# Performance work log

Measured on AMD Instinct MI355X. Metric: run time of the kernel, lower is better.

Reference implementation:

```python
import jax, jax.numpy as jnp
import numpy as np

NH = 8       # num_heads
EDIM = 256   # embedding_dim (also per-head dim in this module)
BS, SQL = 4, 1024


def setup_inputs() -> dict:
    key = jax.random.key(0)
    ks = jax.random.split(key, 5)
    scale_in = 1.0 / np.sqrt(EDIM)
    scale_out = 1.0 / np.sqrt(NH * EDIM)
    return {
        "x": jax.random.normal(ks[0], (BS, SQL, EDIM), dtype=jnp.float32),
        "w_attn": jax.random.normal(ks[1], (NH * 3 * EDIM, EDIM), dtype=jnp.float32) * scale_in,
        "b_attn": jax.random.normal(ks[2], (NH * 3 * EDIM,), dtype=jnp.float32) * scale_in,
        "w_out": jax.random.normal(ks[3], (EDIM, NH * EDIM), dtype=jnp.float32) * scale_out,
        "b_out": jax.random.normal(ks[4], (EDIM,), dtype=jnp.float32) * scale_out,
    }


def reference(x, w_attn, b_attn, w_out, b_out):
    bs, sql, edim = x.shape
    nh = NH
    # projections: (bs, sql, nh*3*edim); split into Q, K, V chunks of nh*edim
    proj = x @ w_attn.T + b_attn
    q, k, v = jnp.split(proj, 3, axis=-1)
    # Faithful to torch: raw view (bs, sql, nh*edim) -> (bs, nh, sql, edim),
    # a reinterpretation of memory, NOT a transpose.
    q = q.reshape(bs, nh, sql, edim)
    k = k.reshape(bs, nh, sql, edim)
    v = v.reshape(bs, nh, sql, edim)
    # scaled dot-product scores: (bs, nh, sql, sql)
    scores = jnp.einsum("bhqd,bhkd->bhqk", q, k) / jnp.sqrt(jnp.float32(edim))
    # causal mask: -inf strictly above the diagonal (equivalent to adding triu(-inf, 1))
    causal = jnp.tril(jnp.ones((sql, sql), dtype=bool))
    scores = jnp.where(causal, scores, -jnp.inf)
    attn = jax.nn.softmax(scores, axis=-1)
    out = jnp.einsum("bhqk,bhkd->bhqd", attn, v)
    # Faithful raw view back: (bs, nh, sql, edim) -> (bs, sql, nh*edim)
    out = out.reshape(bs, sql, nh * edim)
    return out @ w_out.T + b_out
```

## Files before the change

kernel.cpp:

```cpp
#include <hip/hip_runtime.h>

#define SQL  1024
#define EDIM 256
#define NHD  8
#define NKV  (NHD * 3 * EDIM)
#define MROWS (4 * SQL)

typedef short bf16x8 __attribute__((ext_vector_type(8)));
typedef float f32x4 __attribute__((ext_vector_type(4)));

__device__ __forceinline__ unsigned short f2bf(float f) {
  unsigned u = __float_as_uint(f);
  u += 0x7fff + ((u >> 16) & 1);
  return (unsigned short)(u >> 16);
}

__device__ __forceinline__ void g2lds16(const void* g, void* l) {
  __builtin_amdgcn_global_load_lds(
      (const __attribute__((address_space(1))) unsigned int*)g,
      (__attribute__((address_space(3))) unsigned int*)l, 16, 0, 0);
}

__device__ __forceinline__ void storev(float* p, float v) { *p = v; }
__device__ __forceinline__ void storev(unsigned short* p, float v) { *p = f2bf(v); }

__global__ __launch_bounds__(256) void cast_bf16(
    const float* __restrict__ in, unsigned short* __restrict__ out, int n8) {
  int i = blockIdx.x * 256 + threadIdx.x;
  if (i >= n8) return;
  float4 a = ((const float4*)in)[2 * i];
  float4 b = ((const float4*)in)[2 * i + 1];
  union { unsigned short s[8]; ulonglong2 v; } u;
  u.s[0] = f2bf(a.x); u.s[1] = f2bf(a.y); u.s[2] = f2bf(a.z); u.s[3] = f2bf(a.w);
  u.s[4] = f2bf(b.x); u.s[5] = f2bf(b.y); u.s[6] = f2bf(b.z); u.s[7] = f2bf(b.w);
  ((ulonglong2*)out)[i] = u.v;
}

template <int BM, int BN, typename OutT>
__global__ __launch_bounds__(256) void gemm_mfma(
    const unsigned short* __restrict__ A, const unsigned short* __restrict__ B,
    const float* __restrict__ bias, OutT* __restrict__ C,
    int M, int N, int K) {
  constexpr int TM = BM / 32, TN = BN / 32;
  __shared__ __align__(16) unsigned short As[2][BM * 32];
  __shared__ __align__(16) unsigned short Bs[2][BN * 32];
  const int tid = threadIdx.x;
  const int wave = tid >> 6, lane = tid & 63;
  const int quad = lane >> 4, l16 = lane & 15;
  const int wm = (wave >> 1) * (BM / 2), wn = (wave & 1) * (BN / 2);
  const int m0 = blockIdx.x * BM, n0 = blockIdx.y * BN;
  const int sw = (l16 >> 1) & 3;

  f32x4 acc[TM][TN];
  #pragma unroll
  for (int i = 0; i < TM; i++)
    #pragma unroll
    for (int j = 0; j < TN; j++) acc[i][j] = {0.f, 0.f, 0.f, 0.f};

  auto stage = [&](int k0, int bb) {
    #pragma unroll
    for (int it = 0; it < BM / 64; it++) {
      int flat = it * 256 + tid;
      int row = flat >> 2;
      int cg = (flat & 3) ^ ((row >> 1) & 3);
      g2lds16(A + (size_t)(m0 + row) * K + k0 + cg * 8, &As[bb][flat * 8]);
    }
    #pragma unroll
    for (int it = 0; it < BN / 64; it++) {
      int flat = it * 256 + tid;
      int row = flat >> 2;
      int cg = (flat & 3) ^ ((row >> 1) & 3);
      g2lds16(B + (size_t)(n0 + row) * K + k0 + cg * 8, &Bs[bb][flat * 8]);
    }
  };

  stage(0, 0);
  __syncthreads();
  for (int k0 = 0; k0 < K; k0 += 32) {
    const int bb = (k0 >> 5) & 1;
    if (k0 + 32 < K) stage(k0 + 32, bb ^ 1);
    bf16x8 af[TM], bf[TN];
    #pragma unroll
    for (int i = 0; i < TM; i++)
      af[i] = *(const bf16x8*)&As[bb][(wm + i * 16 + l16) * 32 + (quad ^ sw) * 8];
    #pragma unroll
    for (int j = 0; j < TN; j++)
      bf[j] = *(const bf16x8*)&Bs[bb][(wn + j * 16 + l16) * 32 + (quad ^ sw) * 8];
    #pragma unroll
    for (int i = 0; i < TM; i++)
      #pragma unroll
      for (int j = 0; j < TN; j++)
        acc[i][j] = __builtin_amdgcn_mfma_f32_16x16x32_bf16(af[i], bf[j], acc[i][j], 0, 0, 0);
    __syncthreads();
  }

  #pragma unroll
  for (int i = 0; i < TM; i++) {
    #pragma unroll
    for (int r = 0; r < 4; r++) {
      int m = m0 + wm + i * 16 + quad * 4 + r;
      #pragma unroll
      for (int j = 0; j < TN; j++) {
        int n = n0 + wn + j * 16 + l16;
        storev(&C[(size_t)m * N + n], acc[i][j][r] + bias[n]);
      }
    }
  }
}

__global__ __launch_bounds__(256) void transpose_v(
    const unsigned short* __restrict__ proj, unsigned short* __restrict__ vt) {
  __shared__ unsigned short T[64][66];
  const int tid = threadIdx.x;
  const int s0 = blockIdx.x * 64, d0 = blockIdx.y * 64, bh = blockIdx.z;
  const int b = bh >> 3, h = bh & 7;
  #pragma unroll
  for (int it = 0; it < 2; it++) {
    int c = it * 256 + tid;
    int sr = c >> 3, k8 = (c & 7) * 8;
    int s = s0 + sr;
    const unsigned short* src = proj + (size_t)(b * SQL + h * 128 + (s >> 3)) * NKV
                                + 2 * 2048 + (s & 7) * 256 + d0 + k8;
    *(ulonglong2*)&T[sr][k8] = *(const ulonglong2*)src;
  }
  __syncthreads();
  #pragma unroll
  for (int it = 0; it < 2; it++) {
    int c = it * 256 + tid;
    int dr = c >> 3, s8 = (c & 7) * 8;
    unsigned short tmp[8];
    #pragma unroll
    for (int j = 0; j < 8; j++) tmp[j] = T[s8 + j][dr];
    unsigned short* dst = vt + ((size_t)bh * EDIM + d0 + dr) * SQL + s0 + s8;
    *(ulonglong2*)dst = *(ulonglong2*)tmp;
  }
}

__global__ __launch_bounds__(256) void attn_mfma(
    const unsigned short* __restrict__ proj,
    const unsigned short* __restrict__ vt,
    unsigned short* __restrict__ oflat) {
  __shared__ __align__(16) unsigned short lds[35328];
  unsigned short* Ps = lds + 32768;

  const int tid = threadIdx.x;
  const int wave = tid >> 6, lane = tid & 63;
  const int quad = lane >> 4, l16 = lane & 15;
  const int slot = blockIdx.x & 255, round = blockIdx.x >> 8;
  const int bh = slot & 31;
  const int j = slot >> 5;
  const int qt = round ? j : 15 - j;
  const int b = bh >> 3, h = bh & 7;
  const int q0 = qt * 64;

  #pragma unroll
  for (int it = 0; it < 8; it++) {
    int c = it * 256 + tid;
    int r = c >> 5, ch = (c & 31) ^ (r & 7);
    int s = q0 + r;
    g2lds16(proj + (size_t)(b * SQL + h * 128 + (s >> 3)) * NKV + (s & 7) * 256 + ch * 8,
            lds + c * 8);
  }
  __syncthreads();
  bf16x8 aq[8];
  const int qrow = wave * 16 + l16;
  #pragma unroll
  for (int kk = 0; kk < 8; kk++)
    aq[kk] = *(const bf16x8*)&lds[qrow * 256 + ((kk * 4 + quad) ^ (qrow & 7)) * 8];
  __syncthreads();

  f32x4 o[16];
  #pragma unroll
  for (int t = 0; t < 16; t++) o[t] = {0.f, 0.f, 0.f, 0.f};
  float l_r[4] = {0.f, 0.f, 0.f, 0.f};

  auto stage = [&](int kt, int bb) {
    unsigned short* KsB = lds + bb * 16384;
    unsigned short* VtB = KsB + 8192;
    #pragma unroll
    for (int it = 0; it < 4; it++) {
      int c = it * 256 + tid;
      int r = c >> 5, ch = (c & 31) ^ (r & 7);
      int s = kt * 32 + r;
      g2lds16(proj + (size_t)(b * SQL + h * 128 + (s >> 3)) * NKV + 2048 + (s & 7) * 256 + ch * 8,
              KsB + c * 8);
    }
    #pragma unroll
    for (int it = 0; it < 4; it++) {
      int c = it * 256 + tid;
      int d = c >> 2, ch = (c & 3) ^ (d & 3);
      g2lds16(vt + ((size_t)bh * EDIM + d) * SQL + kt * 32 + ch * 8, VtB + c * 8);
    }
  };

  const int nkt = 2 * qt + 2;
  stage(0, 0);
  __syncthreads();

  for (int kt = 0; kt < nkt; kt++) {
    const int bb = kt & 1;
    if (kt + 1 < nkt) stage(kt + 1, bb ^ 1);
    const unsigned short* KsB = lds + bb * 16384;
    const unsigned short* VtB = KsB + 8192;

    f32x4 s0 = {0.f, 0.f, 0.f, 0.f}, s1 = {0.f, 0.f, 0.f, 0.f};
    #pragma unroll
    for (int kk = 0; kk < 8; kk++) {
      int ch = (kk * 4 + quad) ^ (l16 & 7);
      bf16x8 b0 = *(const bf16x8*)&KsB[l16 * 256 + ch * 8];
      bf16x8 b1 = *(const bf16x8*)&KsB[(16 + l16) * 256 + ch * 8];
      s0 = __builtin_amdgcn_mfma_f32_16x16x32_bf16(aq[kk], b0, s0, 0, 0, 0);
      s1 = __builtin_amdgcn_mfma_f32_16x16x32_bf16(aq[kk], b1, s1, 0, 0, 0);
    }

    const int kg0 = kt * 32 + l16, kg1 = kg0 + 16;
    #pragma unroll
    for (int r = 0; r < 4; r++) {
      int qg = q0 + wave * 16 + quad * 4 + r;
      float p0 = (kg0 <= qg) ? __expf(s0[r] * 0.0625f) : 0.f;
      float p1 = (kg1 <= qg) ? __expf(s1[r] * 0.0625f) : 0.f;
      l_r[r] += p0 + p1;
      Ps[(wave * 16 + quad * 4 + r) * 40 + l16]      = f2bf(p0);
      Ps[(wave * 16 + quad * 4 + r) * 40 + 16 + l16] = f2bf(p1);
    }

    bf16x8 ap = *(const bf16x8*)&Ps[(wave * 16 + l16) * 40 + quad * 8];
    #pragma unroll
    for (int t = 0; t < 16; t++) {
      bf16x8 bv = *(const bf16x8*)&VtB[(t * 16 + l16) * 32 + (quad ^ (l16 & 3)) * 8];
      o[t] = __builtin_amdgcn_mfma_f32_16x16x32_bf16(ap, bv, o[t], 0, 0, 0);
    }
    __syncthreads();
  }

  #pragma unroll
  for (int r = 0; r < 4; r++) {
    float l = l_r[r];
    #pragma unroll
    for (int off = 1; off < 16; off <<= 1) l += __shfl_xor(l, off);
    float inv = 1.0f / l;
    int s = q0 + wave * 16 + quad * 4 + r;
    unsigned short* dst = oflat + (size_t)(b * SQL + h * 128 + (s >> 3)) * 2048 + (s & 7) * 256;
    #pragma unroll
    for (int t = 0; t < 16; t++)
      dst[t * 16 + l16] = f2bf(o[t][r] * inv);
  }
}

extern "C" void kernel_launch(void* const* d_in, const int* in_sizes, int n_in,
                              void* d_out, int out_size, void* d_ws, size_t ws_size,
                              hipStream_t stream) {
  const float* x      = (const float*)d_in[0];
  const float* w_attn = (const float*)d_in[1];
  const float* b_attn = (const float*)d_in[2];
  const float* w_out  = (const float*)d_in[3];
  const float* b_out  = (const float*)d_in[4];
  float* out = (float*)d_out;

  char* p = (char*)d_ws;
  unsigned short* proj = (unsigned short*)p;  p += (size_t)MROWS * NKV * 2;
  unsigned short* obf  = (unsigned short*)p;  p += (size_t)MROWS * 2048 * 2;
  unsigned short* vtb  = (unsigned short*)p;  p += (size_t)32 * EDIM * SQL * 2;
  unsigned short* xb   = (unsigned short*)p;  p += (size_t)MROWS * EDIM * 2;
  unsigned short* wb   = (unsigned short*)p;  p += (size_t)NKV * EDIM * 2;
  unsigned short* wob  = (unsigned short*)p;

  cast_bf16<<<(MROWS * EDIM / 8 + 255) / 256, 256, 0, stream>>>(x, xb, MROWS * EDIM / 8);
  cast_bf16<<<(NKV * EDIM / 8 + 255) / 256, 256, 0, stream>>>(w_attn, wb, NKV * EDIM / 8);
  cast_bf16<<<(EDIM * 2048 / 8 + 255) / 256, 256, 0, stream>>>(w_out, wob, EDIM * 2048 / 8);

  gemm_mfma<128, 128, unsigned short><<<dim3(MROWS / 128, NKV / 128), 256, 0, stream>>>(
      xb, wb, b_attn, proj, MROWS, NKV, EDIM);
  transpose_v<<<dim3(SQL / 64, EDIM / 64, 32), 256, 0, stream>>>(proj, vtb);
  attn_mfma<<<512, 256, 0, stream>>>(proj, vtb, obf);
  gemm_mfma<64, 64, float><<<dim3(MROWS / 64, EDIM / 64), 256, 0, stream>>>(
      obf, wob, b_out, out, MROWS, EDIM, NHD * EDIM);
}
```

Measured before the change: 170.9 us.

## Split attention head dim across wave pairs, skip masked tiles, fuse cast kernels

The attention kernel now runs 8 waves per block, with each pair of waves sharing a 16-row query strip and splitting the 256-wide output dimension into two halves. This halves the O accumulator registers per wave and doubles the waves available to hide latency. Waves whose query strip lies entirely before a key tile skip its compute. The exp is rewritten as exp2 with a folded scale constant, and the three fp32-to-bf16 cast launches are merged into one kernel to cut launch overhead. The trade-off is that QK^T is computed twice per query strip, once by each wave of the pair.

```diff
diff --git a/kernel.cpp b/kernel.cpp
--- a/kernel.cpp
+++ b/kernel.cpp
@@ -24,16 +24,21 @@
 __device__ __forceinline__ void storev(float* p, float v) { *p = v; }
 __device__ __forceinline__ void storev(unsigned short* p, float v) { *p = f2bf(v); }
 
-__global__ __launch_bounds__(256) void cast_bf16(
-    const float* __restrict__ in, unsigned short* __restrict__ out, int n8) {
+__global__ __launch_bounds__(256) void cast3_bf16(
+    const float* __restrict__ s0, unsigned short* __restrict__ d0, int n0,
+    const float* __restrict__ s1, unsigned short* __restrict__ d1, int n1,
+    const float* __restrict__ s2, unsigned short* __restrict__ d2, int n2) {
   int i = blockIdx.x * 256 + threadIdx.x;
-  if (i >= n8) return;
-  float4 a = ((const float4*)in)[2 * i];
-  float4 b = ((const float4*)in)[2 * i + 1];
-  union { unsigned short s[8]; ulonglong2 v; } u;
-  u.s[0] = f2bf(a.x); u.s[1] = f2bf(a.y); u.s[2] = f2bf(a.z); u.s[3] = f2bf(a.w);
-  u.s[4] = f2bf(b.x); u.s[5] = f2bf(b.y); u.s[6] = f2bf(b.z); u.s[7] = f2bf(b.w);
-  ((ulonglong2*)out)[i] = u.v;
+  const float* s; unsigned short* d;
+  if (i < n0) { s = s0; d = d0; }
+  else if (i < n0 + n1) { i -= n0; s = s1; d = d1; }
+  else { i -= n0 + n1; if (i >= n2) return; s = s2; d = d2; }
+  float4 a = ((const float4*)s)[2 * i];
+  float4 b = ((const float4*)s)[2 * i + 1];
+  union { unsigned short u[8]; ulonglong2 v; } t;
+  t.u[0] = f2bf(a.x); t.u[1] = f2bf(a.y); t.u[2] = f2bf(a.z); t.u[3] = f2bf(a.w);
+  t.u[4] = f2bf(b.x); t.u[5] = f2bf(b.y); t.u[6] = f2bf(b.z); t.u[7] = f2bf(b.w);
+  ((ulonglong2*)d)[i] = t.v;
 }
 
 template <int BM, int BN, typename OutT>
@@ -136,26 +141,28 @@
   }
 }
 
-__global__ __launch_bounds__(256) void attn_mfma(
+__global__ __launch_bounds__(512, 4) void attn_mfma(
     const unsigned short* __restrict__ proj,
     const unsigned short* __restrict__ vt,
     unsigned short* __restrict__ oflat) {
-  __shared__ __align__(16) unsigned short lds[35328];
+  __shared__ __align__(16) unsigned short lds[37888];
   unsigned short* Ps = lds + 32768;
 
   const int tid = threadIdx.x;
   const int wave = tid >> 6, lane = tid & 63;
   const int quad = lane >> 4, l16 = lane & 15;
+  const int qs = wave >> 1;
+  const int dh = wave & 1;
   const int slot = blockIdx.x & 255, round = blockIdx.x >> 8;
   const int bh = slot & 31;
-  const int j = slot >> 5;
-  const int qt = round ? j : 15 - j;
+  const int jj = slot >> 5;
+  const int qt = round ? jj : 15 - jj;
   const int b = bh >> 3, h = bh & 7;
   const int q0 = qt * 64;
 
   #pragma unroll
-  for (int it = 0; it < 8; it++) {
-    int c = it * 256 + tid;
+  for (int it = 0; it < 4; it++) {
+    int c = it * 512 + tid;
     int r = c >> 5, ch = (c & 31) ^ (r & 7);
     int s = q0 + r;
     g2lds16(proj + (size_t)(b * SQL + h * 128 + (s >> 3)) * NKV + (s & 7) * 256 + ch * 8,
@@ -163,31 +170,31 @@
   }
   __syncthreads();
   bf16x8 aq[8];
-  const int qrow = wave * 16 + l16;
+  const int qrow = qs * 16 + l16;
   #pragma unroll
   for (int kk = 0; kk < 8; kk++)
     aq[kk] = *(const bf16x8*)&lds[qrow * 256 + ((kk * 4 + quad) ^ (qrow & 7)) * 8];
   __syncthreads();
 
-  f32x4 o[16];
-  #pragma unroll
-  for (int t = 0; t < 16; t++) o[t] = {0.f, 0.f, 0.f, 0.f};
+  f32x4 o[8];
+  #pragma unroll
+  for (int t = 0; t < 8; t++) o[t] = {0.f, 0.f, 0.f, 0.f};
   float l_r[4] = {0.f, 0.f, 0.f, 0.f};
 
   auto stage = [&](int kt, int bb) {
     unsigned short* KsB = lds + bb * 16384;
     unsigned short* VtB = KsB + 8192;
     #pragma unroll
-    for (int it = 0; it < 4; it++) {
-      int c = it * 256 + tid;
+    for (int it = 0; it < 2; it++) {
+      int c = it * 512 + tid;
       int r = c >> 5, ch = (c & 31) ^ (r & 7);
       int s = kt * 32 + r;
       g2lds16(proj + (size_t)(b * SQL + h * 128 + (s >> 3)) * NKV + 2048 + (s & 7) * 256 + ch * 8,
               KsB + c * 8);
     }
     #pragma unroll
-    for (int it = 0; it < 4; it++) {
-      int c = it * 256 + tid;
+    for (int it = 0; it < 2; it++) {
+      int c = it * 512 + tid;
       int d = c >> 2, ch = (c & 3) ^ (d & 3);
       g2lds16(vt + ((size_t)bh * EDIM + d) * SQL + kt * 32 + ch * 8, VtB + c * 8);
     }
@@ -202,33 +209,38 @@
     if (kt + 1 < nkt) stage(kt + 1, bb ^ 1);
     const unsigned short* KsB = lds + bb * 16384;
     const unsigned short* VtB = KsB + 8192;
-
-    f32x4 s0 = {0.f, 0.f, 0.f, 0.f}, s1 = {0.f, 0.f, 0.f, 0.f};
-    #pragma unroll
-    for (int kk = 0; kk < 8; kk++) {
-      int ch = (kk * 4 + quad) ^ (l16 & 7);
-      bf16x8 b0 = *(const bf16x8*)&KsB[l16 * 256 + ch * 8];
-      bf16x8 b1 = *(const bf16x8*)&KsB[(16 + l16) * 256 + ch * 8];
-      s0 = __builtin_amdgcn_mfma_f32_16x16x32_bf16(aq[kk], b0, s0, 0, 0, 0);
-      s1 = __builtin_amdgcn_mfma_f32_16x16x32_bf16(aq[kk], b1, s1, 0, 0, 0);
-    }
-
-    const int kg0 = kt * 32 + l16, kg1 = kg0 + 16;
-    #pragma unroll
-    for (int r = 0; r < 4; r++) {
-      int qg = q0 + wave * 16 + quad * 4 + r;
-      float p0 = (kg0 <= qg) ? __expf(s0[r] * 0.0625f) : 0.f;
-      float p1 = (kg1 <= qg) ? __expf(s1[r] * 0.0625f) : 0.f;
-      l_r[r] += p0 + p1;
-      Ps[(wave * 16 + quad * 4 + r) * 40 + l16]      = f2bf(p0);
-      Ps[(wave * 16 + quad * 4 + r) * 40 + 16 + l16] = f2bf(p1);
-    }
-
-    bf16x8 ap = *(const bf16x8*)&Ps[(wave * 16 + l16) * 40 + quad * 8];
-    #pragma unroll
-    for (int t = 0; t < 16; t++) {
-      bf16x8 bv = *(const bf16x8*)&VtB[(t * 16 + l16) * 32 + (quad ^ (l16 & 3)) * 8];
-      o[t] = __builtin_amdgcn_mfma_f32_16x16x32_bf16(ap, bv, o[t], 0, 0, 0);
+    const bool live = (kt * 32 <= q0 + qs * 16 + 15);
+
+    if (live) {
+      f32x4 s0 = {0.f, 0.f, 0.f, 0.f}, s1 = {0.f, 0.f, 0.f, 0.f};
+      #pragma unroll
+      for (int kk = 0; kk < 8; kk++) {
+        int ch = (kk * 4 + quad) ^ (l16 & 7);
+        bf16x8 b0 = *(const bf16x8*)&KsB[l16 * 256 + ch * 8];
+        bf16x8 b1 = *(const bf16x8*)&KsB[(16 + l16) * 256 + ch * 8];
+        s0 = __builtin_amdgcn_mfma_f32_16x16x32_bf16(aq[kk], b0, s0, 0, 0, 0);
+        s1 = __builtin_amdgcn_mfma_f32_16x16x32_bf16(aq[kk], b1, s1, 0, 0, 0);
+      }
+
+      const int kg0 = kt * 32 + l16, kg1 = kg0 + 16;
+      unsigned short* PsW = Ps + wave * 640;
+      #pragma unroll
+      for (int r = 0; r < 4; r++) {
+        int qg = q0 + qs * 16 + quad * 4 + r;
+        float p0 = (kg0 <= qg) ? exp2f(s0[r] * 0.09016844f) : 0.f;
+        float p1 = (kg1 <= qg) ? exp2f(s1[r] * 0.09016844f) : 0.f;
+        l_r[r] += p0 + p1;
+        PsW[(quad * 4 + r) * 40 + l16]      = f2bf(p0);
+        PsW[(quad * 4 + r) * 40 + 16 + l16] = f2bf(p1);
+      }
+
+      bf16x8 ap = *(const bf16x8*)&PsW[l16 * 40 + quad * 8];
+      #pragma unroll
+      for (int tl = 0; tl < 8; tl++) {
+        const int vrow = dh * 128 + tl * 16 + l16;
+        bf16x8 bv = *(const bf16x8*)&VtB[vrow * 32 + (quad ^ (l16 & 3)) * 8];
+        o[tl] = __builtin_amdgcn_mfma_f32_16x16x32_bf16(ap, bv, o[tl], 0, 0, 0);
+      }
     }
     __syncthreads();
   }
@@ -239,11 +251,12 @@
     #pragma unroll
     for (int off = 1; off < 16; off <<= 1) l += __shfl_xor(l, off);
     float inv = 1.0f / l;
-    int s = q0 + wave * 16 + quad * 4 + r;
-    unsigned short* dst = oflat + (size_t)(b * SQL + h * 128 + (s >> 3)) * 2048 + (s & 7) * 256;
-    #pragma unroll
-    for (int t = 0; t < 16; t++)
-      dst[t * 16 + l16] = f2bf(o[t][r] * inv);
+    int s = q0 + qs * 16 + quad * 4 + r;
+    unsigned short* dst = oflat + (size_t)(b * SQL + h * 128 + (s >> 3)) * 2048
+                          + (s & 7) * 256 + dh * 128;
+    #pragma unroll
+    for (int tl = 0; tl < 8; tl++)
+      dst[tl * 16 + l16] = f2bf(o[tl][r] * inv);
   }
 }
 
@@ -265,14 +278,16 @@
   unsigned short* wb   = (unsigned short*)p;  p += (size_t)NKV * EDIM * 2;
   unsigned short* wob  = (unsigned short*)p;
 
-  cast_bf16<<<(MROWS * EDIM / 8 + 255) / 256, 256, 0, stream>>>(x, xb, MROWS * EDIM / 8);
-  cast_bf16<<<(NKV * EDIM / 8 + 255) / 256, 256, 0, stream>>>(w_attn, wb, NKV * EDIM / 8);
-  cast_bf16<<<(EDIM * 2048 / 8 + 255) / 256, 256, 0, stream>>>(w_out, wob, EDIM * 2048 / 8);
+  const int n0 = MROWS * EDIM / 8;
+  const int n1 = NKV * EDIM / 8;
+  const int n2 = EDIM * 2048 / 8;
+  cast3_bf16<<<(n0 + n1 + n2) / 256, 256, 0, stream>>>(x, xb, n0, w_attn, wb, n1,
+                                                       w_out, wob, n2);
 
   gemm_mfma<128, 128, unsigned short><<<dim3(MROWS / 128, NKV / 128), 256, 0, stream>>>(
       xb, wb, b_attn, proj, MROWS, NKV, EDIM);
   transpose_v<<<dim3(SQL / 64, EDIM / 64, 32), 256, 0, stream>>>(proj, vtb);
-  attn_mfma<<<512, 256, 0, stream>>>(proj, vtb, obf);
+  attn_mfma<<<512, 512, 0, stream>>>(proj, vtb, obf);
   gemm_mfma<64, 64, float><<<dim3(MROWS / 64, EDIM / 64), 256, 0, stream>>>(
       obf, wob, b_out, out, MROWS, EDIM, NHD * EDIM);
 }
```

Result: no change. 172.0 us (+0.6%).

## Split-K output projection with atomics and merge three cast kernels into one

Applied to the files above, without the earlier changes.

Replaces the output projection GEMM (K=2048, only 256 blocks) with a split-K version over four K chunks that accumulates into a zeroed output with float atomicAdd, so the GEMM launches more blocks and fills more compute units. The bias is added only by the first K chunk. The three fp32-to-bf16 cast launches are merged into one kernel that picks its source by index range, saving launch overhead. The split-K path adds a memset and atomic traffic, and the summation order is no longer deterministic.

```diff
diff --git a/kernel.cpp b/kernel.cpp
--- a/kernel.cpp
+++ b/kernel.cpp
@@ -24,16 +24,21 @@
 __device__ __forceinline__ void storev(float* p, float v) { *p = v; }
 __device__ __forceinline__ void storev(unsigned short* p, float v) { *p = f2bf(v); }
 
-__global__ __launch_bounds__(256) void cast_bf16(
-    const float* __restrict__ in, unsigned short* __restrict__ out, int n8) {
+__global__ __launch_bounds__(256) void cast3_bf16(
+    const float* __restrict__ s0, unsigned short* __restrict__ d0, int n0,
+    const float* __restrict__ s1, unsigned short* __restrict__ d1, int n1,
+    const float* __restrict__ s2, unsigned short* __restrict__ d2, int n2) {
   int i = blockIdx.x * 256 + threadIdx.x;
-  if (i >= n8) return;
-  float4 a = ((const float4*)in)[2 * i];
-  float4 b = ((const float4*)in)[2 * i + 1];
-  union { unsigned short s[8]; ulonglong2 v; } u;
-  u.s[0] = f2bf(a.x); u.s[1] = f2bf(a.y); u.s[2] = f2bf(a.z); u.s[3] = f2bf(a.w);
-  u.s[4] = f2bf(b.x); u.s[5] = f2bf(b.y); u.s[6] = f2bf(b.z); u.s[7] = f2bf(b.w);
-  ((ulonglong2*)out)[i] = u.v;
+  const float* s; unsigned short* d;
+  if (i < n0) { s = s0; d = d0; }
+  else if (i < n0 + n1) { i -= n0; s = s1; d = d1; }
+  else { i -= n0 + n1; if (i >= n2) return; s = s2; d = d2; }
+  float4 a = ((const float4*)s)[2 * i];
+  float4 b = ((const float4*)s)[2 * i + 1];
+  union { unsigned short u[8]; ulonglong2 v; } t;
+  t.u[0] = f2bf(a.x); t.u[1] = f2bf(a.y); t.u[2] = f2bf(a.z); t.u[3] = f2bf(a.w);
+  t.u[4] = f2bf(b.x); t.u[5] = f2bf(b.y); t.u[6] = f2bf(b.z); t.u[7] = f2bf(b.w);
+  ((ulonglong2*)d)[i] = t.v;
 }
 
 template <int BM, int BN, typename OutT>
@@ -108,6 +113,81 @@
   }
 }
 
+template <int BM, int BN, int KCH>
+__global__ __launch_bounds__(256) void gemm_splitk(
+    const unsigned short* __restrict__ A, const unsigned short* __restrict__ B,
+    const float* __restrict__ bias, float* __restrict__ C,
+    int M, int N, int K) {
+  constexpr int TM = BM / 32, TN = BN / 32;
+  __shared__ __align__(16) unsigned short As[2][BM * 32];
+  __shared__ __align__(16) unsigned short Bs[2][BN * 32];
+  const int tid = threadIdx.x;
+  const int wave = tid >> 6, lane = tid & 63;
+  const int quad = lane >> 4, l16 = lane & 15;
+  const int wm = (wave >> 1) * (BM / 2), wn = (wave & 1) * (BN / 2);
+  const int m0 = blockIdx.x * BM, n0 = blockIdx.y * BN;
+  const int kbase = blockIdx.z * KCH;
+  const int sw = (l16 >> 1) & 3;
+
+  f32x4 acc[TM][TN];
+  #pragma unroll
+  for (int j = 0; j < TN; j++) {
+    const float bb = (blockIdx.z == 0) ? bias[n0 + wn + j * 16 + l16] : 0.f;
+    #pragma unroll
+    for (int i = 0; i < TM; i++) acc[i][j] = {bb, bb, bb, bb};
+  }
+
+  auto stage = [&](int k0, int bb) {
+    #pragma unroll
+    for (int it = 0; it < BM / 64; it++) {
+      int flat = it * 256 + tid;
+      int row = flat >> 2;
+      int cg = (flat & 3) ^ ((row >> 1) & 3);
+      g2lds16(A + (size_t)(m0 + row) * K + k0 + cg * 8, &As[bb][flat * 8]);
+    }
+    #pragma unroll
+    for (int it = 0; it < BN / 64; it++) {
+      int flat = it * 256 + tid;
+      int row = flat >> 2;
+      int cg = (flat & 3) ^ ((row >> 1) & 3);
+      g2lds16(B + (size_t)(n0 + row) * K + k0 + cg * 8, &Bs[bb][flat * 8]);
+    }
+  };
+
+  stage(kbase, 0);
+  __syncthreads();
+  for (int kk = 0; kk < KCH; kk += 32) {
+    const int bb = (kk >> 5) & 1;
+    if (kk + 32 < KCH) stage(kbase + kk + 32, bb ^ 1);
+    bf16x8 af[TM], bf[TN];
+    #pragma unroll
+    for (int i = 0; i < TM; i++)
+      af[i] = *(const bf16x8*)&As[bb][(wm + i * 16 + l16) * 32 + (quad ^ sw) * 8];
+    #pragma unroll
+    for (int j = 0; j < TN; j++)
+      bf[j] = *(const bf16x8*)&Bs[bb][(wn + j * 16 + l16) * 32 + (quad ^ sw) * 8];
+    #pragma unroll
+    for (int i = 0; i < TM; i++)
+      #pragma unroll
+      for (int j = 0; j < TN; j++)
+        acc[i][j] = __builtin_amdgcn_mfma_f32_16x16x32_bf16(af[i], bf[j], acc[i][j], 0, 0, 0);
+    __syncthreads();
+  }
+
+  #pragma unroll
+  for (int i = 0; i < TM; i++) {
+    #pragma unroll
+    for (int r = 0; r < 4; r++) {
+      int m = m0 + wm + i * 16 + quad * 4 + r;
+      #pragma unroll
+      for (int j = 0; j < TN; j++) {
+        int n = n0 + wn + j * 16 + l16;
+        atomicAdd(&C[(size_t)m * N + n], acc[i][j][r]);
+      }
+    }
+  }
+}
+
 __global__ __launch_bounds__(256) void transpose_v(
     const unsigned short* __restrict__ proj, unsigned short* __restrict__ vt) {
   __shared__ unsigned short T[64][66];
@@ -265,14 +345,18 @@
   unsigned short* wb   = (unsigned short*)p;  p += (size_t)NKV * EDIM * 2;
   unsigned short* wob  = (unsigned short*)p;
 
-  cast_bf16<<<(MROWS * EDIM / 8 + 255) / 256, 256, 0, stream>>>(x, xb, MROWS * EDIM / 8);
-  cast_bf16<<<(NKV * EDIM / 8 + 255) / 256, 256, 0, stream>>>(w_attn, wb, NKV * EDIM / 8);
-  cast_bf16<<<(EDIM * 2048 / 8 + 255) / 256, 256, 0, stream>>>(w_out, wob, EDIM * 2048 / 8);
+  const int n0 = MROWS * EDIM / 8;
+  const int n1 = NKV * EDIM / 8;
+  const int n2 = EDIM * 2048 / 8;
+  cast3_bf16<<<(n0 + n1 + n2) / 256, 256, 0, stream>>>(x, xb, n0, w_attn, wb, n1,
+                                                       w_out, wob, n2);
+
+  hipMemsetAsync(out, 0, (size_t)MROWS * EDIM * sizeof(float), stream);
 
   gemm_mfma<128, 128, unsigned short><<<dim3(MROWS / 128, NKV / 128), 256, 0, stream>>>(
       xb, wb, b_attn, proj, MROWS, NKV, EDIM);
   transpose_v<<<dim3(SQL / 64, EDIM / 64, 32), 256, 0, stream>>>(proj, vtb);
   attn_mfma<<<512, 256, 0, stream>>>(proj, vtb, obf);
-  gemm_mfma<64, 64, float><<<dim3(MROWS / 64, EDIM / 64), 256, 0, stream>>>(
+  gemm_splitk<64, 64, 512><<<dim3(MROWS / 64, EDIM / 64, 4), 256, 0, stream>>>(
       obf, wob, b_out, out, MROWS, EDIM, NHD * EDIM);
 }
```

Measured after the change: 168.2 us. Within noise of the previous version (-1.6%).

## Fuse output projection into attention kernel and merge three cast launches

Applied to the files above, without the earlier changes.

Each attention block stages its normalized 64x256 output tile in swizzled LDS. Because of the raw reshape, that tile maps to 8 contiguous rows of the flattened output, so the block multiplies it directly by the bf16 w_out with MFMA, adds the bias and writes fp32 results. This removes the intermediate bf16 attention buffer, its round trip through memory, and the separate output GEMM launch. The three fp32-to-bf16 casts are also merged into one launch. The cost is that each block streams 256x2048 of w_out from global memory with no LDS reuse, and only half the MFMA lanes carry useful rows, which lengthens the attention tail.

```diff
diff --git a/kernel.cpp b/kernel.cpp
--- a/kernel.cpp
+++ b/kernel.cpp
@@ -24,16 +24,21 @@
 __device__ __forceinline__ void storev(float* p, float v) { *p = v; }
 __device__ __forceinline__ void storev(unsigned short* p, float v) { *p = f2bf(v); }
 
-__global__ __launch_bounds__(256) void cast_bf16(
-    const float* __restrict__ in, unsigned short* __restrict__ out, int n8) {
+__global__ __launch_bounds__(256) void cast3_bf16(
+    const float* __restrict__ s0, unsigned short* __restrict__ d0, int n0,
+    const float* __restrict__ s1, unsigned short* __restrict__ d1, int n1,
+    const float* __restrict__ s2, unsigned short* __restrict__ d2, int n2) {
   int i = blockIdx.x * 256 + threadIdx.x;
-  if (i >= n8) return;
-  float4 a = ((const float4*)in)[2 * i];
-  float4 b = ((const float4*)in)[2 * i + 1];
-  union { unsigned short s[8]; ulonglong2 v; } u;
-  u.s[0] = f2bf(a.x); u.s[1] = f2bf(a.y); u.s[2] = f2bf(a.z); u.s[3] = f2bf(a.w);
-  u.s[4] = f2bf(b.x); u.s[5] = f2bf(b.y); u.s[6] = f2bf(b.z); u.s[7] = f2bf(b.w);
-  ((ulonglong2*)out)[i] = u.v;
+  const float* s; unsigned short* d;
+  if (i < n0) { s = s0; d = d0; }
+  else if (i < n0 + n1) { i -= n0; s = s1; d = d1; }
+  else { i -= n0 + n1; if (i >= n2) return; s = s2; d = d2; }
+  float4 a = ((const float4*)s)[2 * i];
+  float4 b = ((const float4*)s)[2 * i + 1];
+  union { unsigned short u[8]; ulonglong2 v; } t;
+  t.u[0] = f2bf(a.x); t.u[1] = f2bf(a.y); t.u[2] = f2bf(a.z); t.u[3] = f2bf(a.w);
+  t.u[4] = f2bf(b.x); t.u[5] = f2bf(b.y); t.u[6] = f2bf(b.z); t.u[7] = f2bf(b.w);
+  ((ulonglong2*)d)[i] = t.v;
 }
 
 template <int BM, int BN, typename OutT>
@@ -139,7 +144,9 @@
 __global__ __launch_bounds__(256) void attn_mfma(
     const unsigned short* __restrict__ proj,
     const unsigned short* __restrict__ vt,
-    unsigned short* __restrict__ oflat) {
+    const unsigned short* __restrict__ wob,
+    const float* __restrict__ b_out,
+    float* __restrict__ out) {
   __shared__ __align__(16) unsigned short lds[35328];
   unsigned short* Ps = lds + 32768;
 
@@ -233,17 +240,51 @@
     __syncthreads();
   }
 
+  float inv[4];
   #pragma unroll
   for (int r = 0; r < 4; r++) {
     float l = l_r[r];
     #pragma unroll
     for (int off = 1; off < 16; off <<= 1) l += __shfl_xor(l, off);
-    float inv = 1.0f / l;
-    int s = q0 + wave * 16 + quad * 4 + r;
-    unsigned short* dst = oflat + (size_t)(b * SQL + h * 128 + (s >> 3)) * 2048 + (s & 7) * 256;
-    #pragma unroll
-    for (int t = 0; t < 16; t++)
-      dst[t * 16 + l16] = f2bf(o[t][r] * inv);
+    inv[r] = 1.0f / l;
+  }
+  unsigned short* Os = lds;
+  const int rr = 2 * wave + (quad >> 1);
+  #pragma unroll
+  for (int t = 0; t < 16; t++) {
+    #pragma unroll
+    for (int r = 0; r < 4; r++) {
+      int c16 = ((quad & 1) * 4 + r) * 32 + t * 2 + (l16 >> 3);
+      Os[rr * 2048 + ((c16 ^ rr) << 3) + (l16 & 7)] = f2bf(o[t][r] * inv[r]);
+    }
+  }
+  __syncthreads();
+
+  f32x4 acc[4];
+  #pragma unroll
+  for (int et = 0; et < 4; et++) {
+    const int e0 = wave * 64 + et * 16 + quad * 4;
+    acc[et] = {b_out[e0], b_out[e0 + 1], b_out[e0 + 2], b_out[e0 + 3]};
+  }
+  const int brow = l16 & 7;
+  #pragma unroll 4
+  for (int kk = 0; kk < 64; kk++) {
+    bf16x8 bo = *(const bf16x8*)&Os[brow * 2048 + (((kk * 4 + quad) ^ brow) << 3)];
+    #pragma unroll
+    for (int et = 0; et < 4; et++) {
+      const unsigned short* wr = wob + ((size_t)(wave * 4 + et) * 16 + l16) * 2048
+                                 + kk * 32 + quad * 8;
+      bf16x8 aw = *(const bf16x8*)wr;
+      acc[et] = __builtin_amdgcn_mfma_f32_16x16x32_bf16(aw, bo, acc[et], 0, 0, 0);
+    }
+  }
+  if (l16 < 8) {
+    const size_t m = (size_t)b * SQL + h * 128 + qt * 8 + l16;
+    #pragma unroll
+    for (int et = 0; et < 4; et++) {
+      float4 v = {acc[et][0], acc[et][1], acc[et][2], acc[et][3]};
+      *(float4*)&out[m * EDIM + wave * 64 + et * 16 + quad * 4] = v;
+    }
   }
 }
 
@@ -259,20 +300,19 @@
 
   char* p = (char*)d_ws;
   unsigned short* proj = (unsigned short*)p;  p += (size_t)MROWS * NKV * 2;
-  unsigned short* obf  = (unsigned short*)p;  p += (size_t)MROWS * 2048 * 2;
   unsigned short* vtb  = (unsigned short*)p;  p += (size_t)32 * EDIM * SQL * 2;
   unsigned short* xb   = (unsigned short*)p;  p += (size_t)MROWS * EDIM * 2;
   unsigned short* wb   = (unsigned short*)p;  p += (size_t)NKV * EDIM * 2;
   unsigned short* wob  = (unsigned short*)p;
 
-  cast_bf16<<<(MROWS * EDIM / 8 + 255) / 256, 256, 0, stream>>>(x, xb, MROWS * EDIM / 8);
-  cast_bf16<<<(NKV * EDIM / 8 + 255) / 256, 256, 0, stream>>>(w_attn, wb, NKV * EDIM / 8);
-  cast_bf16<<<(EDIM * 2048 / 8 + 255) / 256, 256, 0, stream>>>(w_out, wob, EDIM * 2048 / 8);
+  const int n0 = MROWS * EDIM / 8;
+  const int n1 = NKV * EDIM / 8;
+  const int n2 = EDIM * 2048 / 8;
+  cast3_bf16<<<(n0 + n1 + n2) / 256, 256, 0, stream>>>(x, xb, n0, w_attn, wb, n1,
+                                                       w_out, wob, n2);
 
   gemm_mfma<128, 128, unsigned short><<<dim3(MROWS / 128, NKV / 128), 256, 0, stream>>>(
       xb, wb, b_attn, proj, MROWS, NKV, EDIM);
   transpose_v<<<dim3(SQL / 64, EDIM / 64, 32), 256, 0, stream>>>(proj, vtb);
-  attn_mfma<<<512, 256, 0, stream>>>(proj, vtb, obf);
-  gemm_mfma<64, 64, float><<<dim3(MROWS / 64, EDIM / 64), 256, 0, stream>>>(
-      obf, wob, b_out, out, MROWS, EDIM, NHD * EDIM);
-}
+  attn_mfma<<<512, 256, 0, stream>>>(proj, vtb, wob, b_out, out);
+}
```

New measurement: 182.7 us. +6.9%, slower.
